# Performance work log

Measured on AMD Instinct MI355X. Metric: run time of the kernel, lower is better.

Reference implementation:

```python
import jax, jax.numpy as jnp
import numpy as np

B, S, D = 1, 2048, 2048
HQ, HKV, DH = 16, 4, 128
WINDOW = 512  # sliding window encoded in explicit attn_mask


def rotate_half(u):
    u1, u2 = jnp.split(u, 2, axis=-1)
    return jnp.concatenate([-u2, u1], axis=-1)


def setup_inputs() -> dict:
    key = jax.random.key(0)
    ks = jax.random.split(key, 6)
    x = jax.random.normal(ks[0], (B, S, D), dtype=jnp.float32)
    # RoPE caches (standard rotary frequencies, full d_head with duplicated halves)
    pos = jnp.arange(S)
    inv_freq = 1.0 / (10000.0 ** (jnp.arange(0, DH, 2, dtype=jnp.float32) / DH))
    ang = pos[:, None].astype(jnp.float32) * inv_freq[None, :]  # [S, DH/2]
    emb = jnp.concatenate([ang, ang], axis=-1)                  # [S, DH]
    cos_cache = jnp.cos(emb)
    sin_cache = jnp.sin(emb)
    # sliding-window causal mask: attend to j<=i and i-j < WINDOW
    i = jnp.arange(S)[:, None]
    j = jnp.arange(S)[None, :]
    attn_mask = (j <= i) & ((i - j) < WINDOW)
    sc = 0.02
    Wq = jax.random.normal(ks[1], (D, HQ * DH), dtype=jnp.float32) * sc
    Wk = jax.random.normal(ks[2], (D, HKV * DH), dtype=jnp.float32) * sc
    Wv = jax.random.normal(ks[3], (D, HKV * DH), dtype=jnp.float32) * sc
    Wo = jax.random.normal(ks[4], (HQ * DH, D), dtype=jnp.float32) * sc
    return {"x": x, "cos_cache": cos_cache, "sin_cache": sin_cache,
            "positions": pos.astype(jnp.int64), "attn_mask": attn_mask,
            "Wq": Wq, "Wk": Wk, "Wv": Wv, "Wo": Wo}


def reference(x, cos_cache, sin_cache, positions, attn_mask, Wq, Wk, Wv, Wo):
    batch, seq_len, _ = x.shape
    Q = (x @ Wq).reshape(batch, seq_len, HQ, DH).transpose(0, 2, 1, 3)   # [B,HQ,S,DH]
    K = (x @ Wk).reshape(batch, seq_len, HKV, DH).transpose(0, 2, 1, 3)  # [B,HKV,S,DH]
    V = (x @ Wv).reshape(batch, seq_len, HKV, DH).transpose(0, 2, 1, 3)
    # RoPE
    cos = cos_cache[positions][None, None, :, :]  # [1,1,S,DH]
    sin = sin_cache[positions][None, None, :, :]
    Q = Q * cos + rotate_half(Q) * sin
    K = K * cos + rotate_half(K) * sin
    # GQA expansion (repeat_interleave along head dim)
    G = HQ // HKV
    K_exp = jnp.repeat(K, G, axis=1)  # [B,HQ,S,DH]
    V_exp = jnp.repeat(V, G, axis=1)
    scores = jnp.einsum('bhqd,bhkd->bhqk', Q, K_exp) / jnp.sqrt(jnp.float32(DH))
    neg_inf = jnp.finfo(scores.dtype).min
    scores = jnp.where(attn_mask[None, None, :, :], scores, neg_inf)
    weights = jax.nn.softmax(scores, axis=-1)
    attn_out = jnp.einsum('bhqk,bhkd->bhqd', weights, V_exp)
    attn_out = attn_out.transpose(0, 2, 1, 3).reshape(batch, seq_len, HQ * DH)
    output = attn_out @ Wo
    return (output, K, V)  # new kv cache is the (post-RoPE) K, V
```

## Files before the change

kernel.cpp:

```cpp
#include <hip/hip_runtime.h>
#include <stdint.h>

typedef unsigned short u16;
typedef __attribute__((ext_vector_type(4))) float f32x4;
typedef __attribute__((ext_vector_type(8))) short short8;
typedef __attribute__((ext_vector_type(4))) short short4v;

__device__ inline u16 f2bf(float f) {
  union { float f; uint32_t u; } v; v.f = f;
  uint32_t u = v.u;
  u += 0x7fffu + ((u >> 16) & 1u);
  return (u16)(u >> 16);
}
__device__ inline float bf2f(u16 b) {
  union { uint32_t u; float f; } v; v.u = (uint32_t)b << 16; return v.f;
}

__global__ __launch_bounds__(256) void k_prep(const float* __restrict__ x,
                                              const float* __restrict__ Wq, const float* __restrict__ Wk,
                                              const float* __restrict__ Wv, const float* __restrict__ Wo,
                                              u16* __restrict__ xb, u16* __restrict__ WT, u16* __restrict__ WoT) {
  const int b = blockIdx.x, tid = threadIdx.x;
  if (b < 1024) {
    size_t base = (size_t)b * 4096 + tid * 4;
    #pragma unroll
    for (int k = 0; k < 4; ++k) {
      f32x4 v = *(const f32x4*)(x + base + k * 1024);
      short4v o;
      o.x = (short)f2bf(v.x); o.y = (short)f2bf(v.y);
      o.z = (short)f2bf(v.z); o.w = (short)f2bf(v.w);
      *(short4v*)(xb + base + k * 1024) = o;
    }
    return;
  }
  __shared__ float t[64][68];
  const float* W; u16* D; int N, bb;
  if (b < 2048)      { W = Wq; D = WT;                       N = 2048; bb = b - 1024; }
  else if (b < 2304) { W = Wk; D = WT + (size_t)2048 * 2048; N = 512;  bb = b - 2048; }
  else if (b < 2560) { W = Wv; D = WT + (size_t)2560 * 2048; N = 512;  bb = b - 2304; }
  else               { W = Wo; D = WoT;                      N = 2048; bb = b - 2560; }
  const int nb = N >> 6;
  const int n0 = (bb % nb) * 64, k0 = (bb / nb) * 64;
  const int c4 = (tid & 15) * 4, rbase = tid >> 4;
  #pragma unroll
  for (int p = 0; p < 4; ++p) {
    int r = p * 16 + rbase;
    *(f32x4*)&t[r][c4] = *(const f32x4*)&W[(size_t)(k0 + r) * N + n0 + c4];
  }
  __syncthreads();
  const int i = tid >> 2, j = (tid & 3) * 16;
  short8 o0, o1;
  #pragma unroll
  for (int m = 0; m < 8; ++m) o0[m] = (short)f2bf(t[j + m][i]);
  #pragma unroll
  for (int m = 0; m < 8; ++m) o1[m] = (short)f2bf(t[j + 8 + m][i]);
  *(short8*)&D[(size_t)(n0 + i) * 2048 + k0 + j] = o0;
  *(short8*)&D[(size_t)(n0 + i) * 2048 + k0 + j + 8] = o1;
}

__global__ __launch_bounds__(256) void k_gemm64(const u16* __restrict__ A,
                                                const u16* __restrict__ B,
                                                u16* __restrict__ C,
                                                int M, int N, int K) {
  __shared__ u16 As[2][128 * 32];
  __shared__ u16 Bs[2][128 * 32];
  const int tid = threadIdx.x;
  const int wid = tid >> 6, lane = tid & 63;
  const int quad = lane >> 4, l16 = lane & 15;
  const int wm = (wid >> 1) * 64, wn = (wid & 1) * 64;
  const int bm = blockIdx.y * 128, bn = blockIdx.x * 128;
  const int lr = lane >> 2;
  const int lc = (lane & 3) * 8;
  const int kper = K / gridDim.z;
  const int kbeg = blockIdx.z * kper;
  u16* Cz = C + (size_t)blockIdx.z * M * N;

  f32x4 acc[4][4];
  #pragma unroll
  for (int mi = 0; mi < 4; ++mi)
    #pragma unroll
    for (int ni = 0; ni < 4; ++ni)
      acc[mi][ni] = (f32x4){0.f, 0.f, 0.f, 0.f};

  for (int k0 = kbeg; k0 < kbeg + kper; k0 += 64) {
    const u16* Ag = A + (size_t)bm * K + k0;
    const u16* Bg = B + (size_t)bn * K + k0;
    #pragma unroll
    for (int h = 0; h < 2; ++h)
      #pragma unroll
      for (int p = 0; p < 2; ++p) {
        const int r0 = wid * 32 + p * 16;
        const int rr = r0 + lr;
        __builtin_amdgcn_global_load_lds(
            (const __attribute__((address_space(1))) void*)(Ag + (size_t)rr * K + h * 32 + lc),
            (__attribute__((address_space(3))) void*)(&As[h][r0 * 32]),
            16, 0, 0);
        __builtin_amdgcn_global_load_lds(
            (const __attribute__((address_space(1))) void*)(Bg + (size_t)rr * K + h * 32 + lc),
            (__attribute__((address_space(3))) void*)(&Bs[h][r0 * 32]),
            16, 0, 0);
      }
    __syncthreads();
    #pragma unroll
    for (int h = 0; h < 2; ++h) {
      short8 af[4], bfr[4];
      #pragma unroll
      for (int i = 0; i < 4; ++i) {
        af[i]  = *(const short8*)&As[h][(wm + i * 16 + l16) * 32 + quad * 8];
        bfr[i] = *(const short8*)&Bs[h][(wn + i * 16 + l16) * 32 + quad * 8];
      }
      #pragma unroll
      for (int mi = 0; mi < 4; ++mi)
        #pragma unroll
        for (int ni = 0; ni < 4; ++ni)
          acc[mi][ni] = __builtin_amdgcn_mfma_f32_16x16x32_bf16(af[mi], bfr[ni], acc[mi][ni], 0, 0, 0);
    }
    __syncthreads();
  }
  #pragma unroll
  for (int mi = 0; mi < 4; ++mi) {
    int row = bm + wm + mi * 16 + quad * 4;
    #pragma unroll
    for (int ni = 0; ni < 4; ++ni) {
      int col = bn + wn + ni * 16 + l16;
      #pragma unroll
      for (int r = 0; r < 4; ++r)
        Cz[(size_t)(row + r) * N + col] = f2bf(acc[mi][ni][r]);
    }
  }
}

__global__ __launch_bounds__(256) void k_post(const u16* __restrict__ P,
                                              const float* __restrict__ cosc, const float* __restrict__ sinc,
                                              u16* __restrict__ Qb, u16* __restrict__ Kb, u16* __restrict__ Vt,
                                              float* __restrict__ Kout, float* __restrict__ Vout) {
  const size_t st = (size_t)2048 * 3072;
  const int b = blockIdx.x, tid = threadIdx.x;
  if (b < 2048) {
    __shared__ float row[3072];
    const int s = b;
    const u16* p0 = P + (size_t)s * 3072;
    for (int i = tid * 4; i < 3072; i += 1024) {
      short4v a0 = *(const short4v*)(p0 + i);
      short4v a1 = *(const short4v*)(p0 + st + i);
      #pragma unroll
      for (int m = 0; m < 4; ++m)
        row[i + m] = bf2f((u16)a0[m]) + bf2f((u16)a1[m]);
    }
    __syncthreads();
    const int d = tid & 127;
    const int hbase = tid >> 7;
    const float c = cosc[s * 128 + d], sn = sinc[s * 128 + d];
    const float scale = 0.08838834764831845f;
    #pragma unroll
    for (int it = 0; it < 12; ++it) {
      int slice = it * 2 + hbase;
      float v = row[slice * 128 + d];
      if (slice < 20) {
        float other = (d < 64) ? -row[slice * 128 + d + 64] : row[slice * 128 + d - 64];
        float r = v * c + other * sn;
        if (slice < 16) {
          Qb[((size_t)slice * 2048 + s) * 128 + d] = f2bf(r * scale);
        } else {
          int hk = slice - 16;
          Kout[((size_t)hk * 2048 + s) * 128 + d] = r;
          Kb[((size_t)hk * 2048 + s) * 128 + d] = f2bf(r);
        }
      } else {
        int hv = slice - 20;
        Vout[((size_t)hv * 2048 + s) * 128 + d] = v;
      }
    }
  } else {
    __shared__ float t[32][33];
    const int b2 = b - 2048;
    const int c0 = (b2 & 15) * 32, s0 = (b2 >> 4) * 32;
    const int tx = tid & 31, ty = tid >> 5;
    #pragma unroll
    for (int i = ty; i < 32; i += 8) {
      size_t idx = (size_t)(s0 + i) * 3072 + 2560 + c0 + tx;
      t[i][tx] = bf2f(P[idx]) + bf2f(P[st + idx]);
    }
    __syncthreads();
    const int head = c0 >> 7, dbase = c0 & 127;
    #pragma unroll
    for (int i = ty; i < 32; i += 8)
      Vt[((size_t)head * 128 + dbase + i) * 2048 + s0 + tx] = f2bf(t[tx][i]);
  }
}

__global__ __launch_bounds__(256) void k_attn(const u16* __restrict__ Qb,
                                              const u16* __restrict__ Kb,
                                              const u16* __restrict__ Vt,
                                              u16* __restrict__ O) {
  const int qt = blockIdx.x;
  const int hk = blockIdx.y;
  const int tid = threadIdx.x;
  const int wid = tid >> 6, lane = tid & 63;
  const int quad = lane >> 4, l16 = lane & 15;
  const int h = hk * 4 + wid;
  const int qrow0 = qt * 32;
  const u16* Qh = Qb + (size_t)h * 2048 * 128;
  const u16* Kh = Kb + (size_t)hk * 2048 * 128;
  const u16* Vh = Vt + (size_t)hk * 128 * 2048;

  __shared__ u16 Ks[32 * 136];
  __shared__ u16 Vs[128 * 40];
  __shared__ u16 Ps[4][32 * 40];

  short8 qa[2][4];
  #pragma unroll
  for (int mi = 0; mi < 2; ++mi)
    #pragma unroll
    for (int ks = 0; ks < 4; ++ks)
      qa[mi][ks] = *(const short8*)&Qh[(size_t)(qrow0 + mi * 16 + l16) * 128 + ks * 32 + quad * 8];

  f32x4 o[2][8];
  #pragma unroll
  for (int mi = 0; mi < 2; ++mi)
    #pragma unroll
    for (int dt = 0; dt < 8; ++dt) o[mi][dt] = (f32x4){0.f, 0.f, 0.f, 0.f};
  float lsum[2][4] = {{0.f,0.f,0.f,0.f},{0.f,0.f,0.f,0.f}};

  const int c0 = qrow0 > 511 ? (qrow0 - 511) >> 5 : 0;
  const int c1 = (qrow0 + 31) >> 5;

  short8 kreg[2], vreg[2];
  {
    const int jb = c0 * 32;
    #pragma unroll
    for (int i = 0; i < 2; ++i) {
      int lin = i * 256 + tid;
      kreg[i] = *(const short8*)&Kh[(size_t)(jb + (lin >> 4)) * 128 + (lin & 15) * 8];
      vreg[i] = *(const short8*)&Vh[(size_t)(lin >> 2) * 2048 + jb + (lin & 3) * 8];
    }
  }

  for (int c = c0; c <= c1; ++c) {
    const int jbase = c * 32;
    __syncthreads();
    #pragma unroll
    for (int i = 0; i < 2; ++i) {
      int lin = i * 256 + tid;
      *(short8*)&Ks[(lin >> 4) * 136 + (lin & 15) * 8] = kreg[i];
      *(short8*)&Vs[(lin >> 2) * 40  + (lin & 3)  * 8] = vreg[i];
    }
    if (c < c1) {
      const int jb = jbase + 32;
      #pragma unroll
      for (int i = 0; i < 2; ++i) {
        int lin = i * 256 + tid;
        kreg[i] = *(const short8*)&Kh[(size_t)(jb + (lin >> 4)) * 128 + (lin & 15) * 8];
        vreg[i] = *(const short8*)&Vh[(size_t)(lin >> 2) * 2048 + jb + (lin & 3) * 8];
      }
    }
    __syncthreads();

    f32x4 sc[2][2];
    #pragma unroll
    for (int ni = 0; ni < 2; ++ni) {
      sc[0][ni] = (f32x4){0.f, 0.f, 0.f, 0.f};
      sc[1][ni] = (f32x4){0.f, 0.f, 0.f, 0.f};
      #pragma unroll
      for (int ks = 0; ks < 4; ++ks) {
        short8 kf = *(const short8*)&Ks[(ni * 16 + l16) * 136 + ks * 32 + quad * 8];
        sc[0][ni] = __builtin_amdgcn_mfma_f32_16x16x32_bf16(qa[0][ks], kf, sc[0][ni], 0, 0, 0);
        sc[1][ni] = __builtin_amdgcn_mfma_f32_16x16x32_bf16(qa[1][ks], kf, sc[1][ni], 0, 0, 0);
      }
    }
    #pragma unroll
    for (int mi = 0; mi < 2; ++mi) {
      const int rlo = qrow0 + mi * 16;
      #pragma unroll
      for (int ni = 0; ni < 2; ++ni) {
        const int jlo = jbase + ni * 16;
        const bool none = (jlo > rlo + 15) || (jlo + 15 < rlo - 511);
        const bool allv = (jlo + 15 <= rlo) && (jlo >= rlo - 496);
        float p[4];
        if (none) {
          p[0] = p[1] = p[2] = p[3] = 0.f;
        } else if (allv) {
          #pragma unroll
          for (int r = 0; r < 4; ++r) p[r] = __expf(sc[mi][ni][r]);
        } else {
          const int j = jlo + l16;
          #pragma unroll
          for (int r = 0; r < 4; ++r) {
            int i = rlo + quad * 4 + r;
            bool ok = (j <= i) && (i - j < 512);
            p[r] = ok ? __expf(sc[mi][ni][r]) : 0.f;
          }
        }
        #pragma unroll
        for (int r = 0; r < 4; ++r) {
          lsum[mi][r] += p[r];
          Ps[wid][(mi * 16 + quad * 4 + r) * 40 + ni * 16 + l16] = f2bf(p[r]);
        }
      }
    }
    short8 pa[2];
    #pragma unroll
    for (int mi = 0; mi < 2; ++mi)
      pa[mi] = *(const short8*)&Ps[wid][(mi * 16 + l16) * 40 + quad * 8];
    #pragma unroll
    for (int dt = 0; dt < 8; ++dt) {
      short8 vf = *(const short8*)&Vs[(dt * 16 + l16) * 40 + quad * 8];
      o[0][dt] = __builtin_amdgcn_mfma_f32_16x16x32_bf16(pa[0], vf, o[0][dt], 0, 0, 0);
      o[1][dt] = __builtin_amdgcn_mfma_f32_16x16x32_bf16(pa[1], vf, o[1][dt], 0, 0, 0);
    }
  }

  #pragma unroll
  for (int off = 1; off < 16; off <<= 1)
    #pragma unroll
    for (int mi = 0; mi < 2; ++mi)
      #pragma unroll
      for (int r = 0; r < 4; ++r)
        lsum[mi][r] += __shfl_xor(lsum[mi][r], off, 64);
  float inv[2][4];
  #pragma unroll
  for (int mi = 0; mi < 2; ++mi)
    #pragma unroll
    for (int r = 0; r < 4; ++r) inv[mi][r] = 1.0f / lsum[mi][r];

  #pragma unroll
  for (int mi = 0; mi < 2; ++mi)
    #pragma unroll
    for (int dt = 0; dt < 8; ++dt) {
      int col = h * 128 + dt * 16 + l16;
      #pragma unroll
      for (int r = 0; r < 4; ++r) {
        int row = qrow0 + mi * 16 + quad * 4 + r;
        O[(size_t)row * 2048 + col] = f2bf(o[mi][dt][r] * inv[mi][r]);
      }
    }
}

__global__ __launch_bounds__(256) void k_add2(const u16* __restrict__ P, float* __restrict__ C) {
  const size_t st = (size_t)2048 * 2048;
  size_t i = ((size_t)blockIdx.x * 256 + threadIdx.x) * 8;
  short8 a = *(const short8*)(P + i);
  short8 b = *(const short8*)(P + st + i);
  f32x4 lo, hi;
  #pragma unroll
  for (int m = 0; m < 4; ++m)
    lo[m] = bf2f((u16)a[m]) + bf2f((u16)b[m]);
  #pragma unroll
  for (int m = 0; m < 4; ++m)
    hi[m] = bf2f((u16)a[m + 4]) + bf2f((u16)b[m + 4]);
  *(f32x4*)(C + i) = lo;
  *(f32x4*)(C + i + 4) = hi;
}

extern "C" void kernel_launch(void* const* d_in, const int* in_sizes, int n_in,
                              void* d_out, int out_size, void* d_ws, size_t ws_size,
                              hipStream_t stream) {
  const float* x    = (const float*)d_in[0];
  const float* cosc = (const float*)d_in[1];
  const float* sinc = (const float*)d_in[2];
  const float* Wq = (const float*)d_in[5];
  const float* Wk = (const float*)d_in[6];
  const float* Wv = (const float*)d_in[7];
  const float* Wo = (const float*)d_in[8];

  char* ws = (char*)d_ws;
  u16*   xb    = (u16*)(ws);
  u16*   O     = (u16*)(ws);
  u16*   WT    = (u16*)(ws + (8u  << 20));
  u16*   WoT   = (u16*)(ws + (20u << 20));
  u16*   Qb    = (u16*)(ws + (28u << 20));
  u16*   Kb    = (u16*)(ws + (36u << 20));
  u16*   Vt    = (u16*)(ws + (38u << 20));
  u16*   QKVp  = (u16*)(ws + (40u << 20));
  u16*   Op    = (u16*)(ws + (40u << 20));

  float* outO = (float*)d_out;
  float* outK = (float*)d_out + 4194304;
  float* outV = (float*)d_out + 5242880;

  k_prep<<<3584, 256, 0, stream>>>(x, Wq, Wk, Wv, Wo, xb, WT, WoT);
  k_gemm64<<<dim3(24, 16, 2), 256, 0, stream>>>(xb, WT, QKVp, 2048, 3072, 2048);
  k_post<<<3072, 256, 0, stream>>>(QKVp, cosc, sinc, Qb, Kb, Vt, outK, outV);
  k_attn<<<dim3(64, 4), 256, 0, stream>>>(Qb, Kb, Vt, O);
  k_gemm64<<<dim3(16, 16, 2), 256, 0, stream>>>(O, WoT, Op, 2048, 2048, 2048);
  k_add2<<<2048, 256, 0, stream>>>(Op, outO);
}
```

Before: 126.0 us.

## Replace 128x128 GEMM with 256x256 tile, 4-stage LDS pipeline, swizzled LDS

Replaces the 128x128-tile bf16 GEMM with a 256x256-tile, 512-thread kernel. It uses a 4-buffer LDS ring with prefetch two steps ahead, XOR-swizzled LDS layout to avoid bank conflicts, split A/B staging interleaved with MFMA phases, and s_setprio around the MFMA blocks. The output projection now uses split-K of 4 with a 4-way bf16 partial reduction, and the partial buffer moves in the workspace. Larger tiles cut global traffic per FLOP, but they leave fewer blocks (192 and 256) to fill the GPU's CUs and add more bf16 partial rounding.

```diff
diff --git a/kernel.cpp b/kernel.cpp
--- a/kernel.cpp
+++ b/kernel.cpp
@@ -58,67 +58,113 @@
   *(short8*)&D[(size_t)(n0 + i) * 2048 + k0 + j + 8] = o1;
 }
 
-__global__ __launch_bounds__(256) void k_gemm64(const u16* __restrict__ A,
-                                                const u16* __restrict__ B,
-                                                u16* __restrict__ C,
-                                                int M, int N, int K) {
-  __shared__ u16 As[2][128 * 32];
-  __shared__ u16 Bs[2][128 * 32];
+__global__ __launch_bounds__(512, 2) void k_gemm256(const u16* __restrict__ A,
+                                                    const u16* __restrict__ B,
+                                                    u16* __restrict__ C,
+                                                    int M, int N, int K) {
+  __shared__ __align__(16) u16 lds[4 * 16384];
   const int tid = threadIdx.x;
   const int wid = tid >> 6, lane = tid & 63;
   const int quad = lane >> 4, l16 = lane & 15;
-  const int wm = (wid >> 1) * 64, wn = (wid & 1) * 64;
-  const int bm = blockIdx.y * 128, bn = blockIdx.x * 128;
-  const int lr = lane >> 2;
-  const int lc = (lane & 3) * 8;
-  const int kper = K / gridDim.z;
+  const int wm = (wid >> 2) * 128;
+  const int wn = (wid & 3) * 64;
+  const int bm = blockIdx.y * 256, bn = blockIdx.x * 256;
+  const int kper = K / (int)gridDim.z;
+  const int NT = kper >> 5;
   const int kbeg = blockIdx.z * kper;
   u16* Cz = C + (size_t)blockIdx.z * M * N;
 
-  f32x4 acc[4][4];
-  #pragma unroll
-  for (int mi = 0; mi < 4; ++mi)
-    #pragma unroll
-    for (int ni = 0; ni < 4; ++ni)
-      acc[mi][ni] = (f32x4){0.f, 0.f, 0.f, 0.f};
-
-  for (int k0 = kbeg; k0 < kbeg + kper; k0 += 64) {
-    const u16* Ag = A + (size_t)bm * K + k0;
-    const u16* Bg = B + (size_t)bn * K + k0;
-    #pragma unroll
-    for (int h = 0; h < 2; ++h)
-      #pragma unroll
-      for (int p = 0; p < 2; ++p) {
-        const int r0 = wid * 32 + p * 16;
-        const int rr = r0 + lr;
-        __builtin_amdgcn_global_load_lds(
-            (const __attribute__((address_space(1))) void*)(Ag + (size_t)rr * K + h * 32 + lc),
-            (__attribute__((address_space(3))) void*)(&As[h][r0 * 32]),
-            16, 0, 0);
-        __builtin_amdgcn_global_load_lds(
-            (const __attribute__((address_space(1))) void*)(Bg + (size_t)rr * K + h * 32 + lc),
-            (__attribute__((address_space(3))) void*)(&Bs[h][r0 * 32]),
-            16, 0, 0);
-      }
-    __syncthreads();
-    #pragma unroll
-    for (int h = 0; h < 2; ++h) {
-      short8 af[4], bfr[4];
-      #pragma unroll
-      for (int i = 0; i < 4; ++i) {
-        af[i]  = *(const short8*)&As[h][(wm + i * 16 + l16) * 32 + quad * 8];
-        bfr[i] = *(const short8*)&Bs[h][(wn + i * 16 + l16) * 32 + quad * 8];
-      }
-      #pragma unroll
-      for (int mi = 0; mi < 4; ++mi)
-        #pragma unroll
-        for (int ni = 0; ni < 4; ++ni)
-          acc[mi][ni] = __builtin_amdgcn_mfma_f32_16x16x32_bf16(af[mi], bfr[ni], acc[mi][ni], 0, 0, 0);
-    }
-    __syncthreads();
-  }
-  #pragma unroll
-  for (int mi = 0; mi < 4; ++mi) {
+  const int r0 = tid >> 2, pc = tid & 3;
+  const int lc = pc ^ ((r0 >> 1) & 3);
+  const u16* Ag0 = A + (size_t)(bm + r0) * K + kbeg + lc * 8;
+  const u16* Ag1 = A + (size_t)(bm + r0 + 128) * K + kbeg + lc * 8;
+  const u16* Bg0 = B + (size_t)(bn + r0) * K + kbeg + lc * 8;
+  const u16* Bg1 = B + (size_t)(bn + r0 + 128) * K + kbeg + lc * 8;
+  const int d0 = tid * 8, d1 = (tid + 512) * 8;
+
+  auto STAGE_A = [&](int buf, int kt) {
+    __builtin_amdgcn_global_load_lds((const __attribute__((address_space(1))) void*)(Ag0 + kt * 32),
+        (__attribute__((address_space(3))) void*)(&lds[buf * 16384 + d0]), 16, 0, 0);
+    __builtin_amdgcn_global_load_lds((const __attribute__((address_space(1))) void*)(Ag1 + kt * 32),
+        (__attribute__((address_space(3))) void*)(&lds[buf * 16384 + d1]), 16, 0, 0);
+  };
+  auto STAGE_B = [&](int buf, int kt) {
+    __builtin_amdgcn_global_load_lds((const __attribute__((address_space(1))) void*)(Bg0 + kt * 32),
+        (__attribute__((address_space(3))) void*)(&lds[buf * 16384 + 8192 + d0]), 16, 0, 0);
+    __builtin_amdgcn_global_load_lds((const __attribute__((address_space(1))) void*)(Bg1 + kt * 32),
+        (__attribute__((address_space(3))) void*)(&lds[buf * 16384 + 8192 + d1]), 16, 0, 0);
+  };
+  auto LDA = [&](int buf, int mf) -> short8 {
+    const int row = wm + mf * 16 + l16;
+    const int ch = quad ^ ((row >> 1) & 3);
+    return *(const short8*)&lds[buf * 16384 + row * 32 + ch * 8];
+  };
+  auto LDB = [&](int buf, int nf) -> short8 {
+    const int row = wn + nf * 16 + l16;
+    const int ch = quad ^ ((row >> 1) & 3);
+    return *(const short8*)&lds[buf * 16384 + 8192 + row * 32 + ch * 8];
+  };
+
+  f32x4 acc[8][4];
+  #pragma unroll
+  for (int m = 0; m < 8; ++m)
+    #pragma unroll
+    for (int n = 0; n < 4; ++n) acc[m][n] = (f32x4){0.f, 0.f, 0.f, 0.f};
+
+  STAGE_A(0, 0); STAGE_B(0, 0);
+  STAGE_A(1, 1); STAGE_B(1, 1);
+  asm volatile("s_waitcnt vmcnt(4)" ::: "memory");
+  __builtin_amdgcn_s_barrier();
+  asm volatile("" ::: "memory");
+
+  for (int kt = 0; kt < NT; ++kt) {
+    const int c = kt & 3;
+    const bool pre = (kt + 2) < NT;
+    const int pb = (kt + 2) & 3;
+
+    if (pre) STAGE_A(pb, kt + 2);
+    short8 af[4], bf[4];
+    #pragma unroll
+    for (int i = 0; i < 4; ++i) af[i] = LDA(c, i);
+    #pragma unroll
+    for (int i = 0; i < 4; ++i) bf[i] = LDB(c, i);
+    asm volatile("" ::: "memory");
+    __builtin_amdgcn_s_barrier();
+    __builtin_amdgcn_s_setprio(1);
+    #pragma unroll
+    for (int m = 0; m < 4; ++m)
+      #pragma unroll
+      for (int n = 0; n < 4; ++n)
+        acc[m][n] = __builtin_amdgcn_mfma_f32_16x16x32_bf16(af[m], bf[n], acc[m][n], 0, 0, 0);
+    __builtin_amdgcn_s_setprio(0);
+    asm volatile("" ::: "memory");
+    __builtin_amdgcn_s_barrier();
+    asm volatile("" ::: "memory");
+
+    if (pre) STAGE_B(pb, kt + 2);
+    short8 ag[4];
+    #pragma unroll
+    for (int i = 0; i < 4; ++i) ag[i] = LDA(c, 4 + i);
+    asm volatile("" ::: "memory");
+    __builtin_amdgcn_s_barrier();
+    __builtin_amdgcn_s_setprio(1);
+    #pragma unroll
+    for (int m = 0; m < 4; ++m)
+      #pragma unroll
+      for (int n = 0; n < 4; ++n)
+        acc[4 + m][n] = __builtin_amdgcn_mfma_f32_16x16x32_bf16(ag[m], bf[n], acc[4 + m][n], 0, 0, 0);
+    __builtin_amdgcn_s_setprio(0);
+    if (pre) {
+      asm volatile("s_waitcnt vmcnt(4)" ::: "memory");
+    } else if (kt == NT - 2) {
+      asm volatile("s_waitcnt vmcnt(0)" ::: "memory");
+    }
+    __builtin_amdgcn_s_barrier();
+    asm volatile("" ::: "memory");
+  }
+
+  #pragma unroll
+  for (int mi = 0; mi < 8; ++mi) {
     int row = bm + wm + mi * 16 + quad * 4;
     #pragma unroll
     for (int ni = 0; ni < 4; ++ni) {
@@ -336,18 +382,20 @@
     }
 }
 
-__global__ __launch_bounds__(256) void k_add2(const u16* __restrict__ P, float* __restrict__ C) {
+__global__ __launch_bounds__(256) void k_add4(const u16* __restrict__ P, float* __restrict__ C) {
   const size_t st = (size_t)2048 * 2048;
   size_t i = ((size_t)blockIdx.x * 256 + threadIdx.x) * 8;
   short8 a = *(const short8*)(P + i);
   short8 b = *(const short8*)(P + st + i);
+  short8 c = *(const short8*)(P + 2 * st + i);
+  short8 d = *(const short8*)(P + 3 * st + i);
   f32x4 lo, hi;
   #pragma unroll
   for (int m = 0; m < 4; ++m)
-    lo[m] = bf2f((u16)a[m]) + bf2f((u16)b[m]);
+    lo[m] = (bf2f((u16)a[m]) + bf2f((u16)b[m])) + (bf2f((u16)c[m]) + bf2f((u16)d[m]));
   #pragma unroll
   for (int m = 0; m < 4; ++m)
-    hi[m] = bf2f((u16)a[m + 4]) + bf2f((u16)b[m + 4]);
+    hi[m] = (bf2f((u16)a[m + 4]) + bf2f((u16)b[m + 4])) + (bf2f((u16)c[m + 4]) + bf2f((u16)d[m + 4]));
   *(f32x4*)(C + i) = lo;
   *(f32x4*)(C + i + 4) = hi;
 }
@@ -372,16 +420,16 @@
   u16*   Kb    = (u16*)(ws + (36u << 20));
   u16*   Vt    = (u16*)(ws + (38u << 20));
   u16*   QKVp  = (u16*)(ws + (40u << 20));
-  u16*   Op    = (u16*)(ws + (40u << 20));
+  u16*   Op    = (u16*)(ws + (28u << 20));
 
   float* outO = (float*)d_out;
   float* outK = (float*)d_out + 4194304;
   float* outV = (float*)d_out + 5242880;
 
   k_prep<<<3584, 256, 0, stream>>>(x, Wq, Wk, Wv, Wo, xb, WT, WoT);
-  k_gemm64<<<dim3(24, 16, 2), 256, 0, stream>>>(xb, WT, QKVp, 2048, 3072, 2048);
+  k_gemm256<<<dim3(12, 8, 2), 512, 0, stream>>>(xb, WT, QKVp, 2048, 3072, 2048);
   k_post<<<3072, 256, 0, stream>>>(QKVp, cosc, sinc, Qb, Kb, Vt, outK, outV);
   k_attn<<<dim3(64, 4), 256, 0, stream>>>(Qb, Kb, Vt, O);
-  k_gemm64<<<dim3(16, 16, 2), 256, 0, stream>>>(O, WoT, Op, 2048, 2048, 2048);
-  k_add2<<<2048, 256, 0, stream>>>(Op, outO);
-}
+  k_gemm256<<<dim3(8, 8, 4), 512, 0, stream>>>(O, WoT, Op, 2048, 2048, 2048);
+  k_add4<<<2048, 256, 0, stream>>>(Op, outO);
+}
```

Result: no change. 126.3 us (+0.3%).

## Add direct-to-LDS triple-buffered QKV GEMM and split attention rows across more waves

Applied to the files above, without the earlier changes.

Replaces the split-K QKV projection GEMM with a dedicated 128x192-tile kernel that streams A/B tiles straight into LDS via global_load_lds with XOR swizzling and a three-stage buffer ring, removing the partial-sum buffer and its extra reads in the post-processing kernel. The attention kernel now uses 512 threads, with each wave handling 16 query rows instead of 32. This halves per-wave register state and doubles wave parallelism per block. It trades larger LDS use and hand-tuned waitcnt logic for better latency hiding and occupancy.

```diff
diff --git a/kernel.cpp b/kernel.cpp
--- a/kernel.cpp
+++ b/kernel.cpp
@@ -56,6 +56,118 @@
   for (int m = 0; m < 8; ++m) o1[m] = (short)f2bf(t[j + 8 + m][i]);
   *(short8*)&D[(size_t)(n0 + i) * 2048 + k0 + j] = o0;
   *(short8*)&D[(size_t)(n0 + i) * 2048 + k0 + j + 8] = o1;
+}
+
+__global__ __launch_bounds__(512, 2) void k_gemmqkv(const u16* __restrict__ A,
+                                                    const u16* __restrict__ B,
+                                                    u16* __restrict__ C) {
+  const int K = 2048;
+  const int NT = 32;
+  __shared__ __align__(16) u16 lds[3 * 20480];
+  const int tid = threadIdx.x;
+  const int wid = tid >> 6, lane = tid & 63;
+  const int quad = lane >> 4, l16 = lane & 15;
+  const int wm = (wid >> 2) * 64;
+  const int wn = (wid & 3) * 48;
+  const int bm = blockIdx.y * 128, bn = blockIdx.x * 192;
+
+  const u16* aSrc[2]; int aDst[2];
+  #pragma unroll
+  for (int L = 0; L < 2; ++L) {
+    int E = (tid + L * 512) * 8;
+    int r = E >> 6, pc = (E >> 3) & 7;
+    int lc = pc ^ (r & 7);
+    aSrc[L] = A + (size_t)(bm + r) * K + lc * 8;
+    aDst[L] = E;
+  }
+  const u16* bSrc[3]; int bDst[3];
+  #pragma unroll
+  for (int L = 0; L < 3; ++L) {
+    int E = (tid + L * 512) * 8;
+    int r = E >> 6, pc = (E >> 3) & 7;
+    int lc = pc ^ (r & 7);
+    bSrc[L] = B + (size_t)(bn + r) * K + lc * 8;
+    bDst[L] = 8192 + E;
+  }
+
+  #define STAGE(buf, kt) do {                                                              \
+    _Pragma("unroll")                                                                      \
+    for (int L = 0; L < 2; ++L)                                                            \
+      __builtin_amdgcn_global_load_lds(                                                    \
+          (const __attribute__((address_space(1))) void*)(aSrc[L] + (kt) * 64),            \
+          (__attribute__((address_space(3))) void*)(&lds[(buf) * 20480 + aDst[L]]), 16, 0, 0); \
+    _Pragma("unroll")                                                                      \
+    for (int L = 0; L < 3; ++L)                                                            \
+      __builtin_amdgcn_global_load_lds(                                                    \
+          (const __attribute__((address_space(1))) void*)(bSrc[L] + (kt) * 64),            \
+          (__attribute__((address_space(3))) void*)(&lds[(buf) * 20480 + bDst[L]]), 16, 0, 0); \
+  } while (0)
+
+  f32x4 acc[4][3];
+  #pragma unroll
+  for (int m = 0; m < 4; ++m)
+    #pragma unroll
+    for (int n = 0; n < 3; ++n) acc[m][n] = (f32x4){0.f, 0.f, 0.f, 0.f};
+
+  STAGE(0, 0);
+  STAGE(1, 1);
+  asm volatile("s_waitcnt vmcnt(5)" ::: "memory");
+  __builtin_amdgcn_s_barrier();
+
+  int c = 0, p = 2;
+  for (int t = 0; t < NT; ++t) {
+    if (t + 2 < NT) STAGE(p, t + 2);
+
+    short8 af[4][2], bf[3][2];
+    #pragma unroll
+    for (int mf = 0; mf < 4; ++mf)
+      #pragma unroll
+      for (int kc = 0; kc < 2; ++kc) {
+        int R = wm + mf * 16 + l16;
+        int pc = (kc * 4 + quad) ^ (R & 7);
+        af[mf][kc] = *(const short8*)&lds[c * 20480 + R * 64 + pc * 8];
+      }
+    #pragma unroll
+    for (int nf = 0; nf < 3; ++nf)
+      #pragma unroll
+      for (int kc = 0; kc < 2; ++kc) {
+        int Cc = wn + nf * 16 + l16;
+        int pc = (kc * 4 + quad) ^ (Cc & 7);
+        bf[nf][kc] = *(const short8*)&lds[c * 20480 + 8192 + Cc * 64 + pc * 8];
+      }
+
+    __builtin_amdgcn_s_setprio(1);
+    #pragma unroll
+    for (int mf = 0; mf < 4; ++mf)
+      #pragma unroll
+      for (int nf = 0; nf < 3; ++nf)
+        #pragma unroll
+        for (int kc = 0; kc < 2; ++kc)
+          acc[mf][nf] = __builtin_amdgcn_mfma_f32_16x16x32_bf16(af[mf][kc], bf[nf][kc], acc[mf][nf], 0, 0, 0);
+    __builtin_amdgcn_s_setprio(0);
+
+    if (t + 2 < NT) {
+      asm volatile("s_waitcnt vmcnt(5)" ::: "memory");
+    } else if (t + 1 < NT) {
+      asm volatile("s_waitcnt vmcnt(0)" ::: "memory");
+    }
+    __builtin_amdgcn_s_barrier();
+    c = (c == 2) ? 0 : c + 1;
+    p = (p == 2) ? 0 : p + 1;
+  }
+  #undef STAGE
+
+  #pragma unroll
+  for (int mf = 0; mf < 4; ++mf) {
+    int row = bm + wm + mf * 16 + quad * 4;
+    #pragma unroll
+    for (int nf = 0; nf < 3; ++nf) {
+      int col = bn + wn + nf * 16 + l16;
+      #pragma unroll
+      for (int r = 0; r < 4; ++r)
+        C[(size_t)(row + r) * 3072 + col] = f2bf(acc[mf][nf][r]);
+    }
+  }
 }
 
 __global__ __launch_bounds__(256) void k_gemm64(const u16* __restrict__ A,
@@ -134,7 +246,6 @@
                                               const float* __restrict__ cosc, const float* __restrict__ sinc,
                                               u16* __restrict__ Qb, u16* __restrict__ Kb, u16* __restrict__ Vt,
                                               float* __restrict__ Kout, float* __restrict__ Vout) {
-  const size_t st = (size_t)2048 * 3072;
   const int b = blockIdx.x, tid = threadIdx.x;
   if (b < 2048) {
     __shared__ float row[3072];
@@ -142,10 +253,9 @@
     const u16* p0 = P + (size_t)s * 3072;
     for (int i = tid * 4; i < 3072; i += 1024) {
       short4v a0 = *(const short4v*)(p0 + i);
-      short4v a1 = *(const short4v*)(p0 + st + i);
       #pragma unroll
       for (int m = 0; m < 4; ++m)
-        row[i + m] = bf2f((u16)a0[m]) + bf2f((u16)a1[m]);
+        row[i + m] = bf2f((u16)a0[m]);
     }
     __syncthreads();
     const int d = tid & 127;
@@ -179,7 +289,7 @@
     #pragma unroll
     for (int i = ty; i < 32; i += 8) {
       size_t idx = (size_t)(s0 + i) * 3072 + 2560 + c0 + tx;
-      t[i][tx] = bf2f(P[idx]) + bf2f(P[st + idx]);
+      t[i][tx] = bf2f(P[idx]);
     }
     __syncthreads();
     const int head = c0 >> 7, dbase = c0 & 127;
@@ -189,7 +299,7 @@
   }
 }
 
-__global__ __launch_bounds__(256) void k_attn(const u16* __restrict__ Qb,
+__global__ __launch_bounds__(512) void k_attn(const u16* __restrict__ Qb,
                                               const u16* __restrict__ Kb,
                                               const u16* __restrict__ Vt,
                                               u16* __restrict__ O) {
@@ -198,142 +308,111 @@
   const int tid = threadIdx.x;
   const int wid = tid >> 6, lane = tid & 63;
   const int quad = lane >> 4, l16 = lane & 15;
-  const int h = hk * 4 + wid;
+  const int h = hk * 4 + (wid >> 1);
   const int qrow0 = qt * 32;
+  const int r0 = qrow0 + (wid & 1) * 16;
   const u16* Qh = Qb + (size_t)h * 2048 * 128;
   const u16* Kh = Kb + (size_t)hk * 2048 * 128;
   const u16* Vh = Vt + (size_t)hk * 128 * 2048;
 
   __shared__ u16 Ks[32 * 136];
   __shared__ u16 Vs[128 * 40];
-  __shared__ u16 Ps[4][32 * 40];
-
-  short8 qa[2][4];
-  #pragma unroll
-  for (int mi = 0; mi < 2; ++mi)
-    #pragma unroll
-    for (int ks = 0; ks < 4; ++ks)
-      qa[mi][ks] = *(const short8*)&Qh[(size_t)(qrow0 + mi * 16 + l16) * 128 + ks * 32 + quad * 8];
-
-  f32x4 o[2][8];
-  #pragma unroll
-  for (int mi = 0; mi < 2; ++mi)
-    #pragma unroll
-    for (int dt = 0; dt < 8; ++dt) o[mi][dt] = (f32x4){0.f, 0.f, 0.f, 0.f};
-  float lsum[2][4] = {{0.f,0.f,0.f,0.f},{0.f,0.f,0.f,0.f}};
+  __shared__ u16 Ps[8][16 * 40];
+
+  short8 qa[4];
+  #pragma unroll
+  for (int ks = 0; ks < 4; ++ks)
+    qa[ks] = *(const short8*)&Qh[(size_t)(r0 + l16) * 128 + ks * 32 + quad * 8];
+
+  f32x4 o[8];
+  #pragma unroll
+  for (int dt = 0; dt < 8; ++dt) o[dt] = (f32x4){0.f, 0.f, 0.f, 0.f};
+  float lsum[4] = {0.f, 0.f, 0.f, 0.f};
 
   const int c0 = qrow0 > 511 ? (qrow0 - 511) >> 5 : 0;
   const int c1 = (qrow0 + 31) >> 5;
 
-  short8 kreg[2], vreg[2];
+  short8 kreg, vreg;
   {
     const int jb = c0 * 32;
-    #pragma unroll
-    for (int i = 0; i < 2; ++i) {
-      int lin = i * 256 + tid;
-      kreg[i] = *(const short8*)&Kh[(size_t)(jb + (lin >> 4)) * 128 + (lin & 15) * 8];
-      vreg[i] = *(const short8*)&Vh[(size_t)(lin >> 2) * 2048 + jb + (lin & 3) * 8];
-    }
+    kreg = *(const short8*)&Kh[(size_t)(jb + (tid >> 4)) * 128 + (tid & 15) * 8];
+    vreg = *(const short8*)&Vh[(size_t)(tid >> 2) * 2048 + jb + (tid & 3) * 8];
   }
 
   for (int c = c0; c <= c1; ++c) {
     const int jbase = c * 32;
     __syncthreads();
-    #pragma unroll
-    for (int i = 0; i < 2; ++i) {
-      int lin = i * 256 + tid;
-      *(short8*)&Ks[(lin >> 4) * 136 + (lin & 15) * 8] = kreg[i];
-      *(short8*)&Vs[(lin >> 2) * 40  + (lin & 3)  * 8] = vreg[i];
-    }
+    *(short8*)&Ks[(tid >> 4) * 136 + (tid & 15) * 8] = kreg;
+    *(short8*)&Vs[(tid >> 2) * 40  + (tid & 3)  * 8] = vreg;
     if (c < c1) {
       const int jb = jbase + 32;
-      #pragma unroll
-      for (int i = 0; i < 2; ++i) {
-        int lin = i * 256 + tid;
-        kreg[i] = *(const short8*)&Kh[(size_t)(jb + (lin >> 4)) * 128 + (lin & 15) * 8];
-        vreg[i] = *(const short8*)&Vh[(size_t)(lin >> 2) * 2048 + jb + (lin & 3) * 8];
-      }
-    }
-    __syncthreads();
-
-    f32x4 sc[2][2];
+      kreg = *(const short8*)&Kh[(size_t)(jb + (tid >> 4)) * 128 + (tid & 15) * 8];
+      vreg = *(const short8*)&Vh[(size_t)(tid >> 2) * 2048 + jb + (tid & 3) * 8];
+    }
+    __syncthreads();
+
+    f32x4 sc[2];
     #pragma unroll
     for (int ni = 0; ni < 2; ++ni) {
-      sc[0][ni] = (f32x4){0.f, 0.f, 0.f, 0.f};
-      sc[1][ni] = (f32x4){0.f, 0.f, 0.f, 0.f};
+      sc[ni] = (f32x4){0.f, 0.f, 0.f, 0.f};
       #pragma unroll
       for (int ks = 0; ks < 4; ++ks) {
         short8 kf = *(const short8*)&Ks[(ni * 16 + l16) * 136 + ks * 32 + quad * 8];
-        sc[0][ni] = __builtin_amdgcn_mfma_f32_16x16x32_bf16(qa[0][ks], kf, sc[0][ni], 0, 0, 0);
-        sc[1][ni] = __builtin_amdgcn_mfma_f32_16x16x32_bf16(qa[1][ks], kf, sc[1][ni], 0, 0, 0);
-      }
-    }
-    #pragma unroll
-    for (int mi = 0; mi < 2; ++mi) {
-      const int rlo = qrow0 + mi * 16;
-      #pragma unroll
-      for (int ni = 0; ni < 2; ++ni) {
-        const int jlo = jbase + ni * 16;
-        const bool none = (jlo > rlo + 15) || (jlo + 15 < rlo - 511);
-        const bool allv = (jlo + 15 <= rlo) && (jlo >= rlo - 496);
-        float p[4];
-        if (none) {
-          p[0] = p[1] = p[2] = p[3] = 0.f;
-        } else if (allv) {
-          #pragma unroll
-          for (int r = 0; r < 4; ++r) p[r] = __expf(sc[mi][ni][r]);
-        } else {
-          const int j = jlo + l16;
-          #pragma unroll
-          for (int r = 0; r < 4; ++r) {
-            int i = rlo + quad * 4 + r;
-            bool ok = (j <= i) && (i - j < 512);
-            p[r] = ok ? __expf(sc[mi][ni][r]) : 0.f;
-          }
-        }
+        sc[ni] = __builtin_amdgcn_mfma_f32_16x16x32_bf16(qa[ks], kf, sc[ni], 0, 0, 0);
+      }
+    }
+    #pragma unroll
+    for (int ni = 0; ni < 2; ++ni) {
+      const int jlo = jbase + ni * 16;
+      const bool none = (jlo > r0 + 15) || (jlo + 15 < r0 - 511);
+      const bool allv = (jlo + 15 <= r0) && (jlo >= r0 - 496);
+      float p[4];
+      if (none) {
+        p[0] = p[1] = p[2] = p[3] = 0.f;
+      } else if (allv) {
+        #pragma unroll
+        for (int r = 0; r < 4; ++r) p[r] = __expf(sc[ni][r]);
+      } else {
+        const int j = jlo + l16;
         #pragma unroll
         for (int r = 0; r < 4; ++r) {
-          lsum[mi][r] += p[r];
-          Ps[wid][(mi * 16 + quad * 4 + r) * 40 + ni * 16 + l16] = f2bf(p[r]);
+          int i = r0 + quad * 4 + r;
+          bool ok = (j <= i) && (i - j < 512);
+          p[r] = ok ? __expf(sc[ni][r]) : 0.f;
         }
       }
-    }
-    short8 pa[2];
-    #pragma unroll
-    for (int mi = 0; mi < 2; ++mi)
-      pa[mi] = *(const short8*)&Ps[wid][(mi * 16 + l16) * 40 + quad * 8];
+      #pragma unroll
+      for (int r = 0; r < 4; ++r) {
+        lsum[r] += p[r];
+        Ps[wid][(quad * 4 + r) * 40 + ni * 16 + l16] = f2bf(p[r]);
+      }
+    }
+    short8 pa = *(const short8*)&Ps[wid][l16 * 40 + quad * 8];
     #pragma unroll
     for (int dt = 0; dt < 8; ++dt) {
       short8 vf = *(const short8*)&Vs[(dt * 16 + l16) * 40 + quad * 8];
-      o[0][dt] = __builtin_amdgcn_mfma_f32_16x16x32_bf16(pa[0], vf, o[0][dt], 0, 0, 0);
-      o[1][dt] = __builtin_amdgcn_mfma_f32_16x16x32_bf16(pa[1], vf, o[1][dt], 0, 0, 0);
+      o[dt] = __builtin_amdgcn_mfma_f32_16x16x32_bf16(pa, vf, o[dt], 0, 0, 0);
     }
   }
 
   #pragma unroll
   for (int off = 1; off < 16; off <<= 1)
     #pragma unroll
-    for (int mi = 0; mi < 2; ++mi)
-      #pragma unroll
-      for (int r = 0; r < 4; ++r)
-        lsum[mi][r] += __shfl_xor(lsum[mi][r], off, 64);
-  float inv[2][4];
-  #pragma unroll
-  for (int mi = 0; mi < 2; ++mi)
-    #pragma unroll
-    for (int r = 0; r < 4; ++r) inv[mi][r] = 1.0f / lsum[mi][r];
-
-  #pragma unroll
-  for (int mi = 0; mi < 2; ++mi)
-    #pragma unroll
-    for (int dt = 0; dt < 8; ++dt) {
-      int col = h * 128 + dt * 16 + l16;
-      #pragma unroll
-      for (int r = 0; r < 4; ++r) {
-        int row = qrow0 + mi * 16 + quad * 4 + r;
-        O[(size_t)row * 2048 + col] = f2bf(o[mi][dt][r] * inv[mi][r]);
-      }
-    }
+    for (int r = 0; r < 4; ++r)
+      lsum[r] += __shfl_xor(lsum[r], off, 64);
+  float inv[4];
+  #pragma unroll
+  for (int r = 0; r < 4; ++r) inv[r] = 1.0f / lsum[r];
+
+  #pragma unroll
+  for (int dt = 0; dt < 8; ++dt) {
+    int col = h * 128 + dt * 16 + l16;
+    #pragma unroll
+    for (int r = 0; r < 4; ++r) {
+      int row = r0 + quad * 4 + r;
+      O[(size_t)row * 2048 + col] = f2bf(o[dt][r] * inv[r]);
+    }
+  }
 }
 
 __global__ __launch_bounds__(256) void k_add2(const u16* __restrict__ P, float* __restrict__ C) {
@@ -371,7 +450,7 @@
   u16*   Qb    = (u16*)(ws + (28u << 20));
   u16*   Kb    = (u16*)(ws + (36u << 20));
   u16*   Vt    = (u16*)(ws + (38u << 20));
-  u16*   QKVp  = (u16*)(ws + (40u << 20));
+  u16*   QKV   = (u16*)(ws + (40u << 20));
   u16*   Op    = (u16*)(ws + (40u << 20));
 
   float* outO = (float*)d_out;
@@ -379,9 +458,9 @@
   float* outV = (float*)d_out + 5242880;
 
   k_prep<<<3584, 256, 0, stream>>>(x, Wq, Wk, Wv, Wo, xb, WT, WoT);
-  k_gemm64<<<dim3(24, 16, 2), 256, 0, stream>>>(xb, WT, QKVp, 2048, 3072, 2048);
-  k_post<<<3072, 256, 0, stream>>>(QKVp, cosc, sinc, Qb, Kb, Vt, outK, outV);
-  k_attn<<<dim3(64, 4), 256, 0, stream>>>(Qb, Kb, Vt, O);
+  k_gemmqkv<<<dim3(16, 16), 512, 0, stream>>>(xb, WT, QKV);
+  k_post<<<3072, 256, 0, stream>>>(QKV, cosc, sinc, Qb, Kb, Vt, outK, outV);
+  k_attn<<<dim3(64, 4), 512, 0, stream>>>(Qb, Kb, Vt, O);
   k_gemm64<<<dim3(16, 16, 2), 256, 0, stream>>>(O, WoT, Op, 2048, 2048, 2048);
   k_add2<<<2048, 256, 0, stream>>>(Op, outO);
 }
```

Result: faster. 112.4 us (-10.8%).
